# Optimization experiments

Hardware: AMD Instinct MI355X
Metric: run time of the kernel (lower is better)

Reference implementation:

```python
import jax, jax.numpy as jnp
import numpy as np

NV, NR = 30000, 1000
EVV, EVI, EIV = 400000, 120000, 120000
VD, RD, ED = 16, 8, 2
HID, OUT, H1 = 64, 64, 2


def _seg_softmax(logits, seg, n):
    # numerically stable segment softmax over destination nodes
    m = jax.ops.segment_max(logits, seg, num_segments=n)
    m = jnp.where(jnp.isfinite(m), m, 0.0)
    ex = jnp.exp(logits - m[seg])
    den = jax.ops.segment_sum(ex, seg, num_segments=n)
    return ex / (den[seg] + 1e-16)


def _gatv2(x_src, x_dst, src, dst, ea, Wl, Wr, We, att, b, heads, n_dst, concat):
    # PyG GATv2Conv: e = att . leaky_relu(Wl x_j + Wr x_i + We e_ij); out = sum_j softmax(e) * Wl x_j
    C = att.shape[-1]
    hl = (x_src @ Wl).reshape(-1, heads, C)
    hr = (x_dst @ Wr).reshape(-1, heads, C)
    he = (ea @ We).reshape(-1, heads, C)
    xj = hl[src]                                   # [E, H, C]
    g = jax.nn.leaky_relu(xj + hr[dst] + he, 0.2)
    logits = jnp.einsum('ehc,hc->eh', g, att)      # [E, H]
    alpha = _seg_softmax(logits, dst, n_dst)
    out = jax.ops.segment_sum(xj * alpha[..., None], dst, num_segments=n_dst)
    out = out.reshape(n_dst, heads * C) if concat else out.mean(axis=1)
    return out + b


def _self_loops(src, dst, ea, n):
    # PyG add_self_loops(fill_value='mean'): self-loop edge_attr = per-dst mean of incoming edge_attr
    deg = jax.ops.segment_sum(jnp.ones((ea.shape[0],), ea.dtype), dst, num_segments=n)
    mean = jax.ops.segment_sum(ea, dst, num_segments=n) / jnp.maximum(deg, 1.0)[:, None]
    ar = jnp.arange(n, dtype=src.dtype)
    return jnp.concatenate([src, ar]), jnp.concatenate([dst, ar]), jnp.concatenate([ea, mean], axis=0)


def _ln(x, g, b):
    m = x.mean(-1, keepdims=True)
    v = ((x - m) ** 2).mean(-1, keepdims=True)
    return (x - m) * jax.lax.rsqrt(v + 1e-5) * g + b


def setup_inputs() -> dict:
    key = jax.random.key(0)
    ks = iter(jax.random.split(key, 80))
    def rn(shape, s=1.0):
        return jax.random.normal(next(ks), shape, jnp.float32) * s
    def ri(n, hi):
        return jax.random.randint(next(ks), (n,), 0, hi, jnp.int32)
    d = {'x_veh': rn((NV, VD)), 'x_rsu': rn((NR, RD)),
         'ea_v2v': rn((EVV, ED)), 'ea_v2i': rn((EVI, ED)), 'ea_i2v': rn((EIV, ED)),
         'src_v2v': ri(EVV, NV), 'dst_v2v': ri(EVV, NV),
         'src_v2i': ri(EVI, NV), 'dst_v2i': ri(EVI, NR),
         'src_i2v': ri(EIV, NR), 'dst_i2v': ri(EIV, NV)}
    H1C = H1 * HID
    for rel, di_s, di_d in (('vv', VD, VD), ('vi', VD, RD), ('iv', RD, VD)):
        d['Wl_' + rel + '1'] = rn((di_s, H1C), 0.1)
        d['Wr_' + rel + '1'] = rn((di_d, H1C), 0.1)
        d['We_' + rel + '1'] = rn((ED, H1C), 0.1)
        d['att_' + rel + '1'] = rn((H1, HID), 0.1)
        d['b_' + rel + '1'] = jnp.zeros((H1C,), jnp.float32)
    for rel in ('vv', 'vi', 'iv'):
        d['Wl_' + rel + '2'] = rn((H1C, OUT), 0.1)
        d['Wr_' + rel + '2'] = rn((H1C, OUT), 0.1)
        d['We_' + rel + '2'] = rn((ED, OUT), 0.1)
        d['att_' + rel + '2'] = rn((1, OUT), 0.1)
        d['b_' + rel + '2'] = jnp.zeros((OUT,), jnp.float32)
    d['ln_vg'] = jnp.ones((OUT,), jnp.float32)
    d['ln_vb'] = jnp.zeros((OUT,), jnp.float32)
    d['ln_rg'] = jnp.ones((OUT,), jnp.float32)
    d['ln_rb'] = jnp.zeros((OUT,), jnp.float32)
    return d


def reference(x_veh, x_rsu, ea_v2v, ea_v2i, ea_i2v,
              src_v2v, dst_v2v, src_v2i, dst_v2i, src_i2v, dst_i2v,
              Wl_vv1, Wr_vv1, We_vv1, att_vv1, b_vv1,
              Wl_vi1, Wr_vi1, We_vi1, att_vi1, b_vi1,
              Wl_iv1, Wr_iv1, We_iv1, att_iv1, b_iv1,
              Wl_vv2, Wr_vv2, We_vv2, att_vv2, b_vv2,
              Wl_vi2, Wr_vi2, We_vi2, att_vi2, b_vi2,
              Wl_iv2, Wr_iv2, We_iv2, att_iv2, b_iv2,
              ln_vg, ln_vb, ln_rg, ln_rb):
    s_vv, d_vv, ea_vv = _self_loops(src_v2v, dst_v2v, ea_v2v, NV)
    # layer 1 (heads=2, concat=True), HeteroConv aggr='sum'
    v1 = (_gatv2(x_veh, x_veh, s_vv, d_vv, ea_vv, Wl_vv1, Wr_vv1, We_vv1, att_vv1, b_vv1, H1, NV, True)
          + _gatv2(x_rsu, x_veh, src_i2v, dst_i2v, ea_i2v, Wl_iv1, Wr_iv1, We_iv1, att_iv1, b_iv1, H1, NV, True))
    r1 = _gatv2(x_veh, x_rsu, src_v2i, dst_v2i, ea_v2i, Wl_vi1, Wr_vi1, We_vi1, att_vi1, b_vi1, H1, NR, True)
    v1 = jax.nn.elu(v1)
    r1 = jax.nn.elu(r1)
    # layer 2 (heads=1, concat=False -> mean over 1 head)
    v2 = (_gatv2(v1, v1, s_vv, d_vv, ea_vv, Wl_vv2, Wr_vv2, We_vv2, att_vv2, b_vv2, 1, NV, False)
          + _gatv2(r1, v1, src_i2v, dst_i2v, ea_i2v, Wl_iv2, Wr_iv2, We_iv2, att_iv2, b_iv2, 1, NV, False))
    r2 = _gatv2(v1, r1, src_v2i, dst_v2i, ea_v2i, Wl_vi2, Wr_vi2, We_vi2, att_vi2, b_vi2, 1, NR, False)
    return jnp.concatenate([_ln(v2, ln_vg, ln_vb), _ln(r2, ln_rg, ln_rb)], axis=0)
```

## Files before the change

kernel.cpp:

```cpp
#include <hip/hip_runtime.h>
#include <hip/hip_fp16.h>

constexpr int NV = 30000, NR = 1000;
constexpr int EVV = 400000, EVI = 120000, EIV = 120000;
constexpr int ETOT = EVV + EIV + EVI;
constexpr int VB = (NV + 3) / 4;

struct __align__(8) Edge { int s; __half2 ea; };
typedef __half2 h2;

__device__ __forceinline__ h2 h2shfl_xor(h2 v, int m) {
  int i = *(int*)&v;
  i = __shfl_xor(i, m);
  return *(h2*)&i;
}
__device__ __forceinline__ h2 h2max(h2 a, h2 b) {
  h2 r;
  asm("v_pk_max_f16 %0, %1, %2" : "=v"(r) : "v"(a), "v"(b));
  return r;
}

constexpr size_t OFF_CNT_VV = 0;
constexpr size_t OFF_CUR_VV = OFF_CNT_VV + NV;
constexpr size_t OFF_CNT_IV = OFF_CUR_VV + NV;
constexpr size_t OFF_CUR_IV = OFF_CNT_IV + NV;
constexpr size_t OFF_CNT_VI = OFF_CUR_IV + NV;
constexpr size_t OFF_CUR_VI = OFF_CNT_VI + NR;
constexpr size_t ZERO_END   = OFF_CUR_VI + NR;
constexpr size_t OFF_PTR_VV = ZERO_END;
constexpr size_t OFF_PTR_IV = OFF_PTR_VV + NV + 2;
constexpr size_t OFF_PTR_VI = OFF_PTR_IV + NV + 2;
constexpr size_t OFF_E_VV   = OFF_PTR_VI + NR + 2;
constexpr size_t OFF_E_IV   = OFF_E_VV + (size_t)EVV * 2;
constexpr size_t OFF_E_VI   = OFF_E_IV + (size_t)EIV * 2;
constexpr size_t OFF_H      = (OFF_E_VI + (size_t)EVI * 2 + 3) & ~(size_t)3;
constexpr size_t OFF_HL_VV1 = OFF_H;
constexpr size_t OFF_HR_VV1 = OFF_HL_VV1 + (size_t)NV * 64;
constexpr size_t OFF_HR_IV1 = OFF_HR_VV1 + (size_t)NV * 64;
constexpr size_t OFF_HL_VI1 = OFF_HR_IV1 + (size_t)NV * 64;
constexpr size_t OFF_HL_IV1 = OFF_HL_VI1 + (size_t)NV * 64;
constexpr size_t OFF_HR_VI1 = OFF_HL_IV1 + (size_t)NR * 64;
constexpr size_t L1_END     = OFF_HR_VI1 + (size_t)NR * 64;
constexpr size_t OFF_V1     = L1_END;
constexpr size_t OFF_R1     = OFF_V1 + (size_t)NV * 64;
constexpr size_t WS_END     = OFF_R1 + (size_t)NR * 64;
constexpr size_t OFF_HL_VV2 = OFF_H;
constexpr size_t OFF_HR_VV2 = OFF_HL_VV2 + (size_t)NV * 32;
constexpr size_t OFF_HR_IV2 = OFF_HR_VV2 + (size_t)NV * 32;
constexpr size_t OFF_HL_VI2 = OFF_HR_IV2 + (size_t)NV * 32;
constexpr size_t OFF_HL_IV2 = OFF_HL_VI2 + (size_t)NV * 32;
constexpr size_t OFF_HR_VI2 = OFF_HL_IV2 + (size_t)NR * 32;
constexpr size_t L2_END     = OFF_HR_VI2 + (size_t)NR * 32;
static_assert(L2_END <= OFF_V1, "layer-2 overlay must not clobber v1/r1");

__global__ __launch_bounds__(256) void k_count3(
    const int* __restrict__ dvv, const int* __restrict__ div_, const int* __restrict__ dvi,
    int* __restrict__ cvv, int* __restrict__ civ, int* __restrict__ cvi) {
  int t = blockIdx.x * blockDim.x + threadIdx.x;
  if (t < EVV) atomicAdd(&cvv[dvv[t]], 1);
  else if (t < EVV + EIV) atomicAdd(&civ[div_[t - EVV]], 1);
  else if (t < ETOT) atomicAdd(&cvi[dvi[t - EVV - EIV]], 1);
}

__global__ __launch_bounds__(1024) void k_scan3(
    const int* c0, int* p0, int n0,
    const int* c1, int* p1, int n1,
    const int* c2, int* p2, int n2) {
  const int* cnt = blockIdx.x == 0 ? c0 : blockIdx.x == 1 ? c1 : c2;
  int* ptr = blockIdx.x == 0 ? p0 : blockIdx.x == 1 ? p1 : p2;
  int n = blockIdx.x == 0 ? n0 : blockIdx.x == 1 ? n1 : n2;
  __shared__ int tsum[1024];
  int t = threadIdx.x;
  int per = (n + 1023) >> 10;
  int base = t * per;
  int s = 0;
  for (int i = 0; i < per; i++) { int idx = base + i; if (idx < n) s += cnt[idx]; }
  tsum[t] = s;
  for (int off = 1; off < 1024; off <<= 1) {
    __syncthreads();
    int v = (t >= off) ? tsum[t - off] : 0;
    __syncthreads();
    tsum[t] += v;
  }
  __syncthreads();
  int run = tsum[t] - s;
  for (int i = 0; i < per; i++) {
    int idx = base + i;
    if (idx < n) { ptr[idx] = run; run += cnt[idx]; }
  }
  if (t == 1023) ptr[n] = tsum[1023];
}

__global__ __launch_bounds__(256) void k_fill3(
    const int* __restrict__ svv, const int* __restrict__ dvv, const float* __restrict__ eavv,
    const int* __restrict__ siv, const int* __restrict__ div_, const float* __restrict__ eaiv,
    const int* __restrict__ svi, const int* __restrict__ dvi, const float* __restrict__ eavi,
    const int* __restrict__ pvv, int* __restrict__ uvv, Edge* __restrict__ evv,
    const int* __restrict__ piv, int* __restrict__ uiv, Edge* __restrict__ eiv,
    const int* __restrict__ pvi, int* __restrict__ uvi, Edge* __restrict__ evi) {
  int t = blockIdx.x * blockDim.x + threadIdx.x;
  if (t < EVV) {
    int e = t, d = dvv[e];
    int idx = pvv[d] + atomicAdd(&uvv[d], 1);
    Edge ed; ed.s = svv[e]; ed.ea = __floats2half2_rn(eavv[2 * e], eavv[2 * e + 1]);
    evv[idx] = ed;
  } else if (t < EVV + EIV) {
    int e = t - EVV, d = div_[e];
    int idx = piv[d] + atomicAdd(&uiv[d], 1);
    Edge ed; ed.s = siv[e]; ed.ea = __floats2half2_rn(eaiv[2 * e], eaiv[2 * e + 1]);
    eiv[idx] = ed;
  } else if (t < ETOT) {
    int e = t - EVV - EIV, d = dvi[e];
    int idx = pvi[d] + atomicAdd(&uvi[d], 1);
    Edge ed; ed.s = svi[e]; ed.ea = __floats2half2_rn(eavi[2 * e], eavi[2 * e + 1]);
    evi[idx] = ed;
  }
}

template<int K, int NW>
__global__ __launch_bounds__(256) void k_gemm1(const float* __restrict__ X,
    const float* __restrict__ W0, const float* __restrict__ W1,
    const float* __restrict__ W2, const float* __restrict__ W3,
    __half* __restrict__ Y0, __half* __restrict__ Y1,
    __half* __restrict__ Y2, __half* __restrict__ Y3, int n) {
  constexpr int ROWS = 8;
  __shared__ float xs[ROWS][K];
  int r0 = blockIdx.x * ROWS;
  int tid = threadIdx.x;
  int col = tid & 127, grp = tid >> 7;
  for (int i = tid; i < ROWS * K; i += 256) {
    int gi = r0 * K + i;
    ((float*)xs)[i] = (gi < n * K) ? X[gi] : 0.f;
  }
  __syncthreads();
  int oidx = ((col & 63) << 1) + (col >> 6);
#pragma unroll
  for (int rep = 0; rep < NW / 2; rep++) {
    int wi = grp + rep * 2;
    const float* __restrict__ W = wi == 0 ? W0 : wi == 1 ? W1 : wi == 2 ? W2 : W3;
    __half* __restrict__ Y = wi == 0 ? Y0 : wi == 1 ? Y1 : wi == 2 ? Y2 : Y3;
    float acc[ROWS];
#pragma unroll
    for (int r = 0; r < ROWS; r++) acc[r] = 0.f;
#pragma unroll
    for (int k4 = 0; k4 < K / 4; k4++) {
      float w0 = W[(4 * k4 + 0) * 128 + col];
      float w1 = W[(4 * k4 + 1) * 128 + col];
      float w2 = W[(4 * k4 + 2) * 128 + col];
      float w3 = W[(4 * k4 + 3) * 128 + col];
#pragma unroll
      for (int r = 0; r < ROWS; r++) {
        float4 x4 = *(const float4*)&xs[r][4 * k4];
        acc[r] = fmaf(x4.x, w0, acc[r]);
        acc[r] = fmaf(x4.y, w1, acc[r]);
        acc[r] = fmaf(x4.z, w2, acc[r]);
        acc[r] = fmaf(x4.w, w3, acc[r]);
      }
    }
#pragma unroll
    for (int r = 0; r < ROWS; r++)
      if (r0 + r < n) Y[(size_t)(r0 + r) * 128 + oidx] = __float2half(acc[r]);
  }
}

template<int NW>
__global__ __launch_bounds__(64 * NW) void k_gemm2(const __half* __restrict__ X,
    const float* __restrict__ W0, const float* __restrict__ W1,
    const float* __restrict__ W2, const float* __restrict__ W3,
    __half* __restrict__ Y0, __half* __restrict__ Y1,
    __half* __restrict__ Y2, __half* __restrict__ Y3, int n) {
  constexpr int ROWS = 16, K = 128;
  __shared__ float xs[ROWS][K];
  int r0 = blockIdx.x * ROWS;
  int tid = threadIdx.x;
  const __half2* X2 = (const __half2*)X;
  for (int i = tid; i < ROWS * K / 2; i += 64 * NW) {
    int gi = r0 * (K / 2) + i;
    float2 f = (gi < n * (K / 2)) ? __half22float2(X2[gi]) : make_float2(0.f, 0.f);
    ((float*)xs)[2 * i] = f.x;
    ((float*)xs)[2 * i + 1] = f.y;
  }
  __syncthreads();
  int lane = tid & 63, wv = tid >> 6;
  const float* __restrict__ W = wv == 0 ? W0 : wv == 1 ? W1 : wv == 2 ? W2 : W3;
  __half* __restrict__ Y = wv == 0 ? Y0 : wv == 1 ? Y1 : wv == 2 ? Y2 : Y3;
  float acc[ROWS];
#pragma unroll
  for (int r = 0; r < ROWS; r++) acc[r] = 0.f;
  for (int k4 = 0; k4 < K / 4; k4++) {
    float w0 = W[(4 * k4 + 0) * 64 + lane];
    float w1 = W[(4 * k4 + 1) * 64 + lane];
    float w2 = W[(4 * k4 + 2) * 64 + lane];
    float w3 = W[(4 * k4 + 3) * 64 + lane];
#pragma unroll
    for (int r = 0; r < ROWS; r++) {
      float4 x4 = *(const float4*)&xs[r][4 * k4];
      acc[r] = fmaf(x4.x, w0, acc[r]);
      acc[r] = fmaf(x4.y, w1, acc[r]);
      acc[r] = fmaf(x4.z, w2, acc[r]);
      acc[r] = fmaf(x4.w, w3, acc[r]);
    }
  }
#pragma unroll
  for (int r = 0; r < ROWS; r++)
    if (r0 + r < n) Y[(size_t)(r0 + r) * 64 + lane] = __float2half(acc[r]);
}


template<bool SELF>
__device__ __forceinline__ void gatW2(int d, int lane, int eg, int cg,
    int b, int cnt,
    const Edge* __restrict__ ed,
    const __half* __restrict__ hl, const __half* __restrict__ hr,
    const float* __restrict__ We, const float* __restrict__ att,
    float* acc, float& den0, float& den1) {
  h2 hrc2[4], av2[4], w02[4], w12[4];
  {
    float4 r = *(const float4*)&hr[(size_t)d * 128 + cg * 8];
    const h2* hp = (const h2*)&r;
#pragma unroll
    for (int j = 0; j < 4; j++) hrc2[j] = hp[j];
  }
#pragma unroll
  for (int j = 0; j < 4; j++) {
    int c = cg * 4 + j;
    av2[j] = __floats2half2_rn(att[c], att[64 + c]);
    w02[j] = __floats2half2_rn(We[c], We[64 + c]);
    w12[j] = __floats2half2_rn(We[128 + c], We[192 + c]);
  }
  const h2 c02 = __float2half2_rn(0.2f);
  float sum0 = 0.f, sum1 = 0.f;
  auto proc = [&](float4 r, int eab, bool v) {
    const h2* hp = (const h2*)&r;
    h2 eh = *(h2*)&eab;
    h2 ef0 = __low2half2(eh), ef1 = __high2half2(eh);
    h2 lacc = __float2half2_rn(0.f);
#pragma unroll
    for (int j = 0; j < 4; j++) {
      h2 g = __hfma2(ef0, w02[j], __hadd2(hp[j], hrc2[j]));
      g = __hfma2(ef1, w12[j], g);
      h2 lr = h2max(g, __hmul2(c02, g));
      lacc = __hfma2(lr, av2[j], lacc);
    }
#pragma unroll
    for (int o = 1; o <= 8; o <<= 1) lacc = __hadd2(lacc, h2shfl_xor(lacc, o));
    float2 lf = __half22float2(lacc);
    float ex0 = v ? __expf(lf.x) : 0.f;
    float ex1 = v ? __expf(lf.y) : 0.f;
#pragma unroll
    for (int j = 0; j < 4; j++) {
      float2 f = __half22float2(hp[j]);
      acc[2 * j]     = fmaf(ex0, f.x, acc[2 * j]);
      acc[2 * j + 1] = fmaf(ex1, f.y, acc[2 * j + 1]);
    }
    den0 += ex0; den1 += ex1;
  };
  for (int wf = 0; wf < cnt; wf += 64) {
    int idx = wf + lane;
    int es = 0, eab = 0;
    if (idx < cnt) { Edge e = ed[b + idx]; es = e.s; eab = *(const int*)&e.ea; }
    if (SELF) {
      float2 f = __half22float2(*(h2*)&eab);
      sum0 += f.x; sum1 += f.y;
    }
    int wlen = min(64, cnt - wf);
    for (int kk = 0; kk < wlen; kk += 16) {
      int k0 = kk + eg, k1 = kk + 4 + eg, k2 = kk + 8 + eg, k3 = kk + 12 + eg;
      int s0 = __shfl(es, k0), ea0 = __shfl(eab, k0);
      int s1 = __shfl(es, k1), ea1 = __shfl(eab, k1);
      int s2 = __shfl(es, k2), ea2 = __shfl(eab, k2);
      int s3 = __shfl(es, k3), ea3 = __shfl(eab, k3);
      float4 r0 = *(const float4*)&hl[(size_t)s0 * 128 + cg * 8];
      float4 r1 = *(const float4*)&hl[(size_t)s1 * 128 + cg * 8];
      float4 r2 = *(const float4*)&hl[(size_t)s2 * 128 + cg * 8];
      float4 r3 = *(const float4*)&hl[(size_t)s3 * 128 + cg * 8];
      proc(r0, ea0, k0 < wlen);
      proc(r1, ea1, k1 < wlen);
      proc(r2, ea2, k2 < wlen);
      proc(r3, ea3, k3 < wlen);
    }
  }
  if (SELF) {
#pragma unroll
    for (int o = 1; o <= 32; o <<= 1) { sum0 += __shfl_xor(sum0, o); sum1 += __shfl_xor(sum1, o); }
    float dg = fmaxf((float)cnt, 1.f);
    __half2 mh = __floats2half2_rn(sum0 / dg, sum1 / dg);
    int meab = *(const int*)&mh;
    float4 rS = *(const float4*)&hl[(size_t)d * 128 + cg * 8];
    proc(rS, meab, eg == 0);
  }
#pragma unroll
  for (int o = 16; o <= 32; o <<= 1) {
#pragma unroll
    for (int j = 0; j < 8; j++) acc[j] += __shfl_xor(acc[j], o);
    den0 += __shfl_xor(den0, o);
    den1 += __shfl_xor(den1, o);
  }
}

template<bool SELF>
__device__ __forceinline__ void gatW1(int d, int lane, int eg8, int cg8,
    int b, int cnt,
    const Edge* __restrict__ ed,
    const __half* __restrict__ hl, const __half* __restrict__ hr,
    const float* __restrict__ We, const float* __restrict__ att,
    float* acc, float& den) {
  h2 hrc2[4], av2[4], w02[4], w12[4];
  {
    float4 r = *(const float4*)&hr[(size_t)d * 64 + cg8 * 8];
    const h2* hp = (const h2*)&r;
#pragma unroll
    for (int j = 0; j < 4; j++) hrc2[j] = hp[j];
  }
#pragma unroll
  for (int j = 0; j < 4; j++) {
    int c = cg8 * 8 + 2 * j;
    av2[j] = __floats2half2_rn(att[c], att[c + 1]);
    w02[j] = __floats2half2_rn(We[c], We[c + 1]);
    w12[j] = __floats2half2_rn(We[64 + c], We[64 + c + 1]);
  }
  const h2 c02 = __float2half2_rn(0.2f);
  float sum0 = 0.f, sum1 = 0.f;
  auto proc = [&](float4 r, int eab, bool v) {
    const h2* hp = (const h2*)&r;
    h2 eh = *(h2*)&eab;
    h2 ef0 = __low2half2(eh), ef1 = __high2half2(eh);
    h2 lacc = __float2half2_rn(0.f);
#pragma unroll
    for (int j = 0; j < 4; j++) {
      h2 g = __hfma2(ef0, w02[j], __hadd2(hp[j], hrc2[j]));
      g = __hfma2(ef1, w12[j], g);
      h2 lr = h2max(g, __hmul2(c02, g));
      lacc = __hfma2(lr, av2[j], lacc);
    }
#pragma unroll
    for (int o = 1; o <= 4; o <<= 1) lacc = __hadd2(lacc, h2shfl_xor(lacc, o));
    float2 lf = __half22float2(lacc);
    float ex = v ? __expf(lf.x + lf.y) : 0.f;
#pragma unroll
    for (int j = 0; j < 4; j++) {
      float2 f = __half22float2(hp[j]);
      acc[2 * j]     = fmaf(ex, f.x, acc[2 * j]);
      acc[2 * j + 1] = fmaf(ex, f.y, acc[2 * j + 1]);
    }
    den += ex;
  };
  for (int wf = 0; wf < cnt; wf += 64) {
    int idx = wf + lane;
    int es = 0, eab = 0;
    if (idx < cnt) { Edge e = ed[b + idx]; es = e.s; eab = *(const int*)&e.ea; }
    if (SELF) {
      float2 f = __half22float2(*(h2*)&eab);
      sum0 += f.x; sum1 += f.y;
    }
    int wlen = min(64, cnt - wf);
    for (int kk = 0; kk < wlen; kk += 32) {
      int k0 = kk + eg8, k1 = kk + 8 + eg8, k2 = kk + 16 + eg8, k3 = kk + 24 + eg8;
      int s0 = __shfl(es, k0), ea0 = __shfl(eab, k0);
      int s1 = __shfl(es, k1), ea1 = __shfl(eab, k1);
      int s2 = __shfl(es, k2), ea2 = __shfl(eab, k2);
      int s3 = __shfl(es, k3), ea3 = __shfl(eab, k3);
      float4 r0 = *(const float4*)&hl[(size_t)s0 * 64 + cg8 * 8];
      float4 r1 = *(const float4*)&hl[(size_t)s1 * 64 + cg8 * 8];
      float4 r2 = *(const float4*)&hl[(size_t)s2 * 64 + cg8 * 8];
      float4 r3 = *(const float4*)&hl[(size_t)s3 * 64 + cg8 * 8];
      proc(r0, ea0, k0 < wlen);
      proc(r1, ea1, k1 < wlen);
      proc(r2, ea2, k2 < wlen);
      proc(r3, ea3, k3 < wlen);
    }
  }
  if (SELF) {
#pragma unroll
    for (int o = 1; o <= 32; o <<= 1) { sum0 += __shfl_xor(sum0, o); sum1 += __shfl_xor(sum1, o); }
    float dg = fmaxf((float)cnt, 1.f);
    __half2 mh = __floats2half2_rn(sum0 / dg, sum1 / dg);
    int meab = *(const int*)&mh;
    float4 rS = *(const float4*)&hl[(size_t)d * 64 + cg8 * 8];
    proc(rS, meab, eg8 == 0);
  }
#pragma unroll
  for (int o = 8; o <= 32; o <<= 1) {
#pragma unroll
    for (int j = 0; j < 8; j++) acc[j] += __shfl_xor(acc[j], o);
    den += __shfl_xor(den, o);
  }
}

__global__ __launch_bounds__(256) void k_gat_l1(
    const int* ptr_vv, const Edge* e_vv,
    const __half* hl_vv, const __half* hr_vv, const float* We_vv, const float* att_vv,
    const int* ptr_iv, const Edge* e_iv,
    const __half* hl_iv, const __half* hr_iv, const float* We_iv, const float* att_iv,
    const int* ptr_vi, const Edge* e_vi,
    const __half* hl_vi, const __half* hr_vi, const float* We_vi, const float* att_vi,
    const float* b_vv, const float* b_iv, const float* b_vi,
    __half* __restrict__ v1, __half* __restrict__ r1) {
  __shared__ float sm[4][16][10];
  int lane = threadIdx.x & 63, wv = threadIdx.x >> 6;
  int eg = lane >> 4, cg = lane & 15;
  if (blockIdx.x >= NR) {
    int w = (blockIdx.x - NR) * 4 + wv;
    if (w >= NV) return;
    float acc[8] = {0, 0, 0, 0, 0, 0, 0, 0};
    float d0 = 0.f, d1 = 0.f, oc[8];
    int b = ptr_vv[w], cnt = ptr_vv[w + 1] - b;
    gatW2<true>(w, lane, eg, cg, b, cnt, e_vv, hl_vv, hr_vv, We_vv, att_vv, acc, d0, d1);
#pragma unroll
    for (int j = 0; j < 8; j++) oc[j] = acc[j] / (((j & 1) ? d1 : d0) + 1e-16f);
#pragma unroll
    for (int j = 0; j < 8; j++) acc[j] = 0.f;
    d0 = d1 = 0.f;
    b = ptr_iv[w]; cnt = ptr_iv[w + 1] - b;
    gatW2<false>(w, lane, eg, cg, b, cnt, e_iv, hl_iv, hr_iv, We_iv, att_iv, acc, d0, d1);
#pragma unroll
    for (int j = 0; j < 8; j++) oc[j] += acc[j] / (((j & 1) ? d1 : d0) + 1e-16f);
    if (eg == 0) {
      float x[8];
#pragma unroll
      for (int j = 0; j < 8; j++) {
        int c = cg * 4 + (j >> 1);
        int idx = (j & 1) * 64 + c;
        float v = oc[j] + b_vv[idx] + b_iv[idx];
        x[j] = v > 0.f ? v : __expf(v) - 1.f;
      }
      __half2 h0a = __floats2half2_rn(x[0], x[2]), h0b = __floats2half2_rn(x[4], x[6]);
      __half2 h1a = __floats2half2_rn(x[1], x[3]), h1b = __floats2half2_rn(x[5], x[7]);
      float2 p0, p1;
      ((__half2*)&p0)[0] = h0a; ((__half2*)&p0)[1] = h0b;
      ((__half2*)&p1)[0] = h1a; ((__half2*)&p1)[1] = h1b;
      *(float2*)&v1[(size_t)w * 128 + cg * 4]      = p0;
      *(float2*)&v1[(size_t)w * 128 + 64 + cg * 4] = p1;
    }
  } else {
    int dd = blockIdx.x;
    int bfull = ptr_vi[dd], cntf = ptr_vi[dd + 1] - bfull;
    int q = (cntf + 3) >> 2;
    int off = min(wv * q, cntf);
    int cnt = min(q, cntf - off);
    float acc[8] = {0, 0, 0, 0, 0, 0, 0, 0};
    float d0 = 0.f, d1 = 0.f;
    gatW2<false>(dd, lane, eg, cg, bfull + off, cnt, e_vi, hl_vi, hr_vi, We_vi, att_vi, acc, d0, d1);
    if (eg == 0) {
#pragma unroll
      for (int j = 0; j < 8; j++) sm[wv][cg][j] = acc[j];
      sm[wv][cg][8] = d0; sm[wv][cg][9] = d1;
    }
    __syncthreads();
    if (wv == 0) {
#pragma unroll
      for (int j = 0; j < 8; j++)
        acc[j] = sm[0][cg][j] + sm[1][cg][j] + sm[2][cg][j] + sm[3][cg][j];
      d0 = sm[0][cg][8] + sm[1][cg][8] + sm[2][cg][8] + sm[3][cg][8];
      d1 = sm[0][cg][9] + sm[1][cg][9] + sm[2][cg][9] + sm[3][cg][9];
      if (eg == 0) {
        float x[8];
#pragma unroll
        for (int j = 0; j < 8; j++) {
          int c = cg * 4 + (j >> 1);
          int idx = (j & 1) * 64 + c;
          float v = acc[j] / (((j & 1) ? d1 : d0) + 1e-16f) + b_vi[idx];
          x[j] = v > 0.f ? v : __expf(v) - 1.f;
        }
        __half2 h0a = __floats2half2_rn(x[0], x[2]), h0b = __floats2half2_rn(x[4], x[6]);
        __half2 h1a = __floats2half2_rn(x[1], x[3]), h1b = __floats2half2_rn(x[5], x[7]);
        float2 p0, p1;
        ((__half2*)&p0)[0] = h0a; ((__half2*)&p0)[1] = h0b;
        ((__half2*)&p1)[0] = h1a; ((__half2*)&p1)[1] = h1b;
        *(float2*)&r1[(size_t)dd * 128 + cg * 4]      = p0;
        *(float2*)&r1[(size_t)dd * 128 + 64 + cg * 4] = p1;
      }
    }
  }
}

__global__ __launch_bounds__(256) void k_gat_l2(
    const int* ptr_vv, const Edge* e_vv,
    const __half* hl_vv, const __half* hr_vv, const float* We_vv, const float* att_vv,
    const int* ptr_iv, const Edge* e_iv,
    const __half* hl_iv, const __half* hr_iv, const float* We_iv, const float* att_iv,
    const int* ptr_vi, const Edge* e_vi,
    const __half* hl_vi, const __half* hr_vi, const float* We_vi, const float* att_vi,
    const float* b_vv, const float* b_iv, const float* b_vi,
    const float* ln_vg, const float* ln_vb, const float* ln_rg, const float* ln_rb,
    float* __restrict__ out) {
  __shared__ float sm[4][8][9];
  int lane = threadIdx.x & 63, wv = threadIdx.x >> 6;
  int eg8 = lane >> 3, cg8 = lane & 7;
  if (blockIdx.x >= NR) {
    int w = (blockIdx.x - NR) * 4 + wv;
    if (w >= NV) return;
    float acc[8] = {0, 0, 0, 0, 0, 0, 0, 0};
    float dn = 0.f, oc[8];
    int b = ptr_vv[w], cnt = ptr_vv[w + 1] - b;
    gatW1<true>(w, lane, eg8, cg8, b, cnt, e_vv, hl_vv, hr_vv, We_vv, att_vv, acc, dn);
#pragma unroll
    for (int j = 0; j < 8; j++) oc[j] = acc[j] / (dn + 1e-16f);
#pragma unroll
    for (int j = 0; j < 8; j++) acc[j] = 0.f;
    dn = 0.f;
    b = ptr_iv[w]; cnt = ptr_iv[w + 1] - b;
    gatW1<false>(w, lane, eg8, cg8, b, cnt, e_iv, hl_iv, hr_iv, We_iv, att_iv, acc, dn);
    float x[8], s = 0.f;
#pragma unroll
    for (int j = 0; j < 8; j++) {
      int c = cg8 * 8 + j;
      x[j] = oc[j] + acc[j] / (dn + 1e-16f) + b_vv[c] + b_iv[c];
      s += x[j];
    }
#pragma unroll
    for (int o = 1; o <= 4; o <<= 1) s += __shfl_xor(s, o);
    float mu = s * (1.f / 64.f);
    float v = 0.f;
#pragma unroll
    for (int j = 0; j < 8; j++) { float dx = x[j] - mu; v = fmaf(dx, dx, v); }
#pragma unroll
    for (int o = 1; o <= 4; o <<= 1) v += __shfl_xor(v, o);
    float rstd = rsqrtf(v * (1.f / 64.f) + 1e-5f);
    if (eg8 == 0) {
      float4 o0, o1;
      float* ov = (float*)&o0;
#pragma unroll
      for (int j = 0; j < 4; j++) {
        int c = cg8 * 8 + j;
        ov[j] = (x[j] - mu) * rstd * ln_vg[c] + ln_vb[c];
      }
      ov = (float*)&o1;
#pragma unroll
      for (int j = 0; j < 4; j++) {
        int c = cg8 * 8 + 4 + j;
        ov[j] = (x[4 + j] - mu) * rstd * ln_vg[c] + ln_vb[c];
      }
      *(float4*)&out[(size_t)w * 64 + cg8 * 8]     = o0;
      *(float4*)&out[(size_t)w * 64 + cg8 * 8 + 4] = o1;
    }
  } else {
    int dd = blockIdx.x;
    int bfull = ptr_vi[dd], cntf = ptr_vi[dd + 1] - bfull;
    int q = (cntf + 3) >> 2;
    int off = min(wv * q, cntf);
    int cnt = min(q, cntf - off);
    float acc[8] = {0, 0, 0, 0, 0, 0, 0, 0};
    float dn = 0.f;
    gatW1<false>(dd, lane, eg8, cg8, bfull + off, cnt, e_vi, hl_vi, hr_vi, We_vi, att_vi, acc, dn);
    if (eg8 == 0) {
#pragma unroll
      for (int j = 0; j < 8; j++) sm[wv][cg8][j] = acc[j];
      sm[wv][cg8][8] = dn;
    }
    __syncthreads();
    if (wv == 0) {
#pragma unroll
      for (int j = 0; j < 8; j++)
        acc[j] = sm[0][cg8][j] + sm[1][cg8][j] + sm[2][cg8][j] + sm[3][cg8][j];
      dn = sm[0][cg8][8] + sm[1][cg8][8] + sm[2][cg8][8] + sm[3][cg8][8];
      float x[8], s = 0.f;
#pragma unroll
      for (int j = 0; j < 8; j++) {
        int c = cg8 * 8 + j;
        x[j] = acc[j] / (dn + 1e-16f) + b_vi[c];
        s += x[j];
      }
#pragma unroll
      for (int o = 1; o <= 4; o <<= 1) s += __shfl_xor(s, o);
      float mu = s * (1.f / 64.f);
      float v = 0.f;
#pragma unroll
      for (int j = 0; j < 8; j++) { float dx = x[j] - mu; v = fmaf(dx, dx, v); }
#pragma unroll
      for (int o = 1; o <= 4; o <<= 1) v += __shfl_xor(v, o);
      float rstd = rsqrtf(v * (1.f / 64.f) + 1e-5f);
      if (eg8 == 0) {
#pragma unroll
        for (int j = 0; j < 8; j++) {
          int c = cg8 * 8 + j;
          out[(size_t)(NV + dd) * 64 + c] = (x[j] - mu) * rstd * ln_rg[c] + ln_rb[c];
        }
      }
    }
  }
}

extern "C" void kernel_launch(void* const* d_in, const int* in_sizes, int n_in,
                              void* d_out, int out_size, void* d_ws, size_t ws_size,
                              hipStream_t stream) {
  const float* x_veh  = (const float*)d_in[0];
  const float* x_rsu  = (const float*)d_in[1];
  const float* ea_vv  = (const float*)d_in[2];
  const float* ea_vi  = (const float*)d_in[3];
  const float* ea_iv  = (const float*)d_in[4];
  const int*   src_vv = (const int*)d_in[5];
  const int*   dst_vv = (const int*)d_in[6];
  const int*   src_vi = (const int*)d_in[7];
  const int*   dst_vi = (const int*)d_in[8];
  const int*   src_iv = (const int*)d_in[9];
  const int*   dst_iv = (const int*)d_in[10];
  const float* Wl_vv1 = (const float*)d_in[11];
  const float* Wr_vv1 = (const float*)d_in[12];
  const float* We_vv1 = (const float*)d_in[13];
  const float* att_vv1= (const float*)d_in[14];
  const float* b_vv1  = (const float*)d_in[15];
  const float* Wl_vi1 = (const float*)d_in[16];
  const float* Wr_vi1 = (const float*)d_in[17];
  const float* We_vi1 = (const float*)d_in[18];
  const float* att_vi1= (const float*)d_in[19];
  const float* b_vi1  = (const float*)d_in[20];
  const float* Wl_iv1 = (const float*)d_in[21];
  const float* Wr_iv1 = (const float*)d_in[22];
  const float* We_iv1 = (const float*)d_in[23];
  const float* att_iv1= (const float*)d_in[24];
  const float* b_iv1  = (const float*)d_in[25];
  const float* Wl_vv2 = (const float*)d_in[26];
  const float* Wr_vv2 = (const float*)d_in[27];
  const float* We_vv2 = (const float*)d_in[28];
  const float* att_vv2= (const float*)d_in[29];
  const float* b_vv2  = (const float*)d_in[30];
  const float* Wl_vi2 = (const float*)d_in[31];
  const float* Wr_vi2 = (const float*)d_in[32];
  const float* We_vi2 = (const float*)d_in[33];
  const float* att_vi2= (const float*)d_in[34];
  const float* b_vi2  = (const float*)d_in[35];
  const float* Wl_iv2 = (const float*)d_in[36];
  const float* Wr_iv2 = (const float*)d_in[37];
  const float* We_iv2 = (const float*)d_in[38];
  const float* att_iv2= (const float*)d_in[39];
  const float* b_iv2  = (const float*)d_in[40];
  const float* ln_vg  = (const float*)d_in[41];
  const float* ln_vb  = (const float*)d_in[42];
  const float* ln_rg  = (const float*)d_in[43];
  const float* ln_rb  = (const float*)d_in[44];

  float* ws  = (float*)d_ws;
  float* out = (float*)d_out;

  int* cnt_vv = (int*)(ws + OFF_CNT_VV); int* cur_vv = (int*)(ws + OFF_CUR_VV);
  int* cnt_iv = (int*)(ws + OFF_CNT_IV); int* cur_iv = (int*)(ws + OFF_CUR_IV);
  int* cnt_vi = (int*)(ws + OFF_CNT_VI); int* cur_vi = (int*)(ws + OFF_CUR_VI);
  int* ptr_vv = (int*)(ws + OFF_PTR_VV);
  int* ptr_iv = (int*)(ws + OFF_PTR_IV);
  int* ptr_vi = (int*)(ws + OFF_PTR_VI);
  Edge* e_vv = (Edge*)(ws + OFF_E_VV);
  Edge* e_iv = (Edge*)(ws + OFF_E_IV);
  Edge* e_vi = (Edge*)(ws + OFF_E_VI);

  __half* hl_vv1 = (__half*)(ws + OFF_HL_VV1);
  __half* hr_vv1 = (__half*)(ws + OFF_HR_VV1);
  __half* hr_iv1 = (__half*)(ws + OFF_HR_IV1);
  __half* hl_vi1 = (__half*)(ws + OFF_HL_VI1);
  __half* hl_iv1 = (__half*)(ws + OFF_HL_IV1);
  __half* hr_vi1 = (__half*)(ws + OFF_HR_VI1);
  __half* v1 = (__half*)(ws + OFF_V1);
  __half* r1 = (__half*)(ws + OFF_R1);
  __half* hl_vv2 = (__half*)(ws + OFF_HL_VV2);
  __half* hr_vv2 = (__half*)(ws + OFF_HR_VV2);
  __half* hr_iv2 = (__half*)(ws + OFF_HR_IV2);
  __half* hl_vi2 = (__half*)(ws + OFF_HL_VI2);
  __half* hl_iv2 = (__half*)(ws + OFF_HL_IV2);
  __half* hr_vi2 = (__half*)(ws + OFF_HR_VI2);

  (void)hipMemsetAsync(ws, 0, ZERO_END * sizeof(float), stream);

  k_count3<<<(ETOT + 255) / 256, 256, 0, stream>>>(dst_vv, dst_iv, dst_vi,
      cnt_vv, cnt_iv, cnt_vi);
  k_scan3<<<3, 1024, 0, stream>>>(cnt_vv, ptr_vv, NV, cnt_iv, ptr_iv, NV, cnt_vi, ptr_vi, NR);
  k_fill3<<<(ETOT + 255) / 256, 256, 0, stream>>>(
      src_vv, dst_vv, ea_vv, src_iv, dst_iv, ea_iv, src_vi, dst_vi, ea_vi,
      ptr_vv, cur_vv, e_vv, ptr_iv, cur_iv, e_iv, ptr_vi, cur_vi, e_vi);

  k_gemm1<16, 4><<<(NV + 7) / 8, 256, 0, stream>>>(x_veh,
      Wl_vv1, Wr_vv1, Wr_iv1, Wl_vi1, hl_vv1, hr_vv1, hr_iv1, hl_vi1, NV);
  k_gemm1<8, 2><<<(NR + 7) / 8, 256, 0, stream>>>(x_rsu,
      Wl_iv1, Wr_vi1, nullptr, nullptr, hl_iv1, hr_vi1, nullptr, nullptr, NR);

  k_gat_l1<<<NR + VB, 256, 0, stream>>>(
      ptr_vv, e_vv, hl_vv1, hr_vv1, We_vv1, att_vv1,
      ptr_iv, e_iv, hl_iv1, hr_iv1, We_iv1, att_iv1,
      ptr_vi, e_vi, hl_vi1, hr_vi1, We_vi1, att_vi1,
      b_vv1, b_iv1, b_vi1, v1, r1);

  k_gemm2<4><<<(NV + 15) / 16, 256, 0, stream>>>(v1,
      Wl_vv2, Wr_vv2, Wr_iv2, Wl_vi2, hl_vv2, hr_vv2, hr_iv2, hl_vi2, NV);
  k_gemm2<2><<<(NR + 15) / 16, 128, 0, stream>>>(r1,
      Wl_iv2, Wr_vi2, nullptr, nullptr, hl_iv2, hr_vi2, nullptr, nullptr, NR);

  k_gat_l2<<<NR + VB, 256, 0, stream>>>(
      ptr_vv, e_vv, hl_vv2, hr_vv2, We_vv2, att_vv2,
      ptr_iv, e_iv, hl_iv2, hr_iv2, We_iv2, att_iv2,
      ptr_vi, e_vi, hl_vi2, hr_vi2, We_vi2, att_vi2,
      b_vv2, b_iv2, b_vi2, ln_vg, ln_vb, ln_rg, ln_rb, out);
  (void)in_sizes; (void)n_in; (void)out_size; (void)ws_size;
}
```

Measured before the change: 365.0 us.

## Accumulate weighted messages in packed fp16 and split edge loop into full and tail

The per-edge weighted accumulation of source features moves from eight fp32 FMAs to four packed fp16 FMAs. The exponent is shifted by a constant offset so the fp16 accumulators stay in range, and the cross-lane reduction now shuffles half2 values. The edge loop is split into an unpredicated main body that handles four edges per group and a one-edge tail, which cuts the validity checks. This lowers ALU and register cost in the aggregation, but fp16 accumulation can lose precision or overflow on high-degree nodes or large logits.

```diff
diff --git a/kernel.cpp b/kernel.cpp
--- a/kernel.cpp
+++ b/kernel.cpp
@@ -5,6 +5,7 @@
 constexpr int EVV = 400000, EVI = 120000, EIV = 120000;
 constexpr int ETOT = EVV + EIV + EVI;
 constexpr int VB = (NV + 3) / 4;
+constexpr float LOFF = 4.0f;
 
 struct __align__(8) Edge { int s; __half2 ea; };
 typedef __half2 h2;
@@ -229,6 +230,9 @@
     w12[j] = __floats2half2_rn(We[128 + c], We[192 + c]);
   }
   const h2 c02 = __float2half2_rn(0.2f);
+  h2 acc2[4];
+#pragma unroll
+  for (int j = 0; j < 4; j++) acc2[j] = __float2half2_rn(0.f);
   float sum0 = 0.f, sum1 = 0.f;
   auto proc = [&](float4 r, int eab, bool v) {
     const h2* hp = (const h2*)&r;
@@ -245,14 +249,11 @@
 #pragma unroll
     for (int o = 1; o <= 8; o <<= 1) lacc = __hadd2(lacc, h2shfl_xor(lacc, o));
     float2 lf = __half22float2(lacc);
-    float ex0 = v ? __expf(lf.x) : 0.f;
-    float ex1 = v ? __expf(lf.y) : 0.f;
-#pragma unroll
-    for (int j = 0; j < 4; j++) {
-      float2 f = __half22float2(hp[j]);
-      acc[2 * j]     = fmaf(ex0, f.x, acc[2 * j]);
-      acc[2 * j + 1] = fmaf(ex1, f.y, acc[2 * j + 1]);
-    }
+    float ex0 = v ? __expf(lf.x - LOFF) : 0.f;
+    float ex1 = v ? __expf(lf.y - LOFF) : 0.f;
+    h2 exh = __floats2half2_rn(ex0, ex1);
+#pragma unroll
+    for (int j = 0; j < 4; j++) acc2[j] = __hfma2(exh, hp[j], acc2[j]);
     den0 += ex0; den1 += ex1;
   };
   for (int wf = 0; wf < cnt; wf += 64) {
@@ -264,7 +265,8 @@
       sum0 += f.x; sum1 += f.y;
     }
     int wlen = min(64, cnt - wf);
-    for (int kk = 0; kk < wlen; kk += 16) {
+    int kk = 0;
+    for (; kk + 16 <= wlen; kk += 16) {
       int k0 = kk + eg, k1 = kk + 4 + eg, k2 = kk + 8 + eg, k3 = kk + 12 + eg;
       int s0 = __shfl(es, k0), ea0 = __shfl(eab, k0);
       int s1 = __shfl(es, k1), ea1 = __shfl(eab, k1);
@@ -274,10 +276,16 @@
       float4 r1 = *(const float4*)&hl[(size_t)s1 * 128 + cg * 8];
       float4 r2 = *(const float4*)&hl[(size_t)s2 * 128 + cg * 8];
       float4 r3 = *(const float4*)&hl[(size_t)s3 * 128 + cg * 8];
+      proc(r0, ea0, true);
+      proc(r1, ea1, true);
+      proc(r2, ea2, true);
+      proc(r3, ea3, true);
+    }
+    for (; kk < wlen; kk += 4) {
+      int k0 = kk + eg;
+      int s0 = __shfl(es, k0), ea0 = __shfl(eab, k0);
+      float4 r0 = *(const float4*)&hl[(size_t)s0 * 128 + cg * 8];
       proc(r0, ea0, k0 < wlen);
-      proc(r1, ea1, k1 < wlen);
-      proc(r2, ea2, k2 < wlen);
-      proc(r3, ea3, k3 < wlen);
     }
   }
   if (SELF) {
@@ -292,9 +300,14 @@
 #pragma unroll
   for (int o = 16; o <= 32; o <<= 1) {
 #pragma unroll
-    for (int j = 0; j < 8; j++) acc[j] += __shfl_xor(acc[j], o);
+    for (int j = 0; j < 4; j++) acc2[j] = __hadd2(acc2[j], h2shfl_xor(acc2[j], o));
     den0 += __shfl_xor(den0, o);
     den1 += __shfl_xor(den1, o);
+  }
+#pragma unroll
+  for (int j = 0; j < 4; j++) {
+    float2 f = __half22float2(acc2[j]);
+    acc[2 * j] = f.x; acc[2 * j + 1] = f.y;
   }
 }
 
@@ -320,6 +333,9 @@
     w12[j] = __floats2half2_rn(We[64 + c], We[64 + c + 1]);
   }
   const h2 c02 = __float2half2_rn(0.2f);
+  h2 acc2[4];
+#pragma unroll
+  for (int j = 0; j < 4; j++) acc2[j] = __float2half2_rn(0.f);
   float sum0 = 0.f, sum1 = 0.f;
   auto proc = [&](float4 r, int eab, bool v) {
     const h2* hp = (const h2*)&r;
@@ -336,13 +352,10 @@
 #pragma unroll
     for (int o = 1; o <= 4; o <<= 1) lacc = __hadd2(lacc, h2shfl_xor(lacc, o));
     float2 lf = __half22float2(lacc);
-    float ex = v ? __expf(lf.x + lf.y) : 0.f;
-#pragma unroll
-    for (int j = 0; j < 4; j++) {
-      float2 f = __half22float2(hp[j]);
-      acc[2 * j]     = fmaf(ex, f.x, acc[2 * j]);
-      acc[2 * j + 1] = fmaf(ex, f.y, acc[2 * j + 1]);
-    }
+    float ex = v ? __expf(lf.x + lf.y - LOFF) : 0.f;
+    h2 exh = __float2half2_rn(ex);
+#pragma unroll
+    for (int j = 0; j < 4; j++) acc2[j] = __hfma2(exh, hp[j], acc2[j]);
     den += ex;
   };
   for (int wf = 0; wf < cnt; wf += 64) {
@@ -354,7 +367,8 @@
       sum0 += f.x; sum1 += f.y;
     }
     int wlen = min(64, cnt - wf);
-    for (int kk = 0; kk < wlen; kk += 32) {
+    int kk = 0;
+    for (; kk + 32 <= wlen; kk += 32) {
       int k0 = kk + eg8, k1 = kk + 8 + eg8, k2 = kk + 16 + eg8, k3 = kk + 24 + eg8;
       int s0 = __shfl(es, k0), ea0 = __shfl(eab, k0);
       int s1 = __shfl(es, k1), ea1 = __shfl(eab, k1);
@@ -364,10 +378,16 @@
       float4 r1 = *(const float4*)&hl[(size_t)s1 * 64 + cg8 * 8];
       float4 r2 = *(const float4*)&hl[(size_t)s2 * 64 + cg8 * 8];
       float4 r3 = *(const float4*)&hl[(size_t)s3 * 64 + cg8 * 8];
+      proc(r0, ea0, true);
+      proc(r1, ea1, true);
+      proc(r2, ea2, true);
+      proc(r3, ea3, true);
+    }
+    for (; kk < wlen; kk += 8) {
+      int k0 = kk + eg8;
+      int s0 = __shfl(es, k0), ea0 = __shfl(eab, k0);
+      float4 r0 = *(const float4*)&hl[(size_t)s0 * 64 + cg8 * 8];
       proc(r0, ea0, k0 < wlen);
-      proc(r1, ea1, k1 < wlen);
-      proc(r2, ea2, k2 < wlen);
-      proc(r3, ea3, k3 < wlen);
     }
   }
   if (SELF) {
@@ -382,8 +402,13 @@
 #pragma unroll
   for (int o = 8; o <= 32; o <<= 1) {
 #pragma unroll
-    for (int j = 0; j < 8; j++) acc[j] += __shfl_xor(acc[j], o);
+    for (int j = 0; j < 4; j++) acc2[j] = __hadd2(acc2[j], h2shfl_xor(acc2[j], o));
     den += __shfl_xor(den, o);
+  }
+#pragma unroll
+  for (int j = 0; j < 4; j++) {
+    float2 f = __half22float2(acc2[j]);
+    acc[2 * j] = f.x; acc[2 * j + 1] = f.y;
   }
 }
 
@@ -402,14 +427,12 @@
   if (blockIdx.x >= NR) {
     int w = (blockIdx.x - NR) * 4 + wv;
     if (w >= NV) return;
-    float acc[8] = {0, 0, 0, 0, 0, 0, 0, 0};
+    float acc[8];
     float d0 = 0.f, d1 = 0.f, oc[8];
     int b = ptr_vv[w], cnt = ptr_vv[w + 1] - b;
     gatW2<true>(w, lane, eg, cg, b, cnt, e_vv, hl_vv, hr_vv, We_vv, att_vv, acc, d0, d1);
 #pragma unroll
     for (int j = 0; j < 8; j++) oc[j] = acc[j] / (((j & 1) ? d1 : d0) + 1e-16f);
-#pragma unroll
-    for (int j = 0; j < 8; j++) acc[j] = 0.f;
     d0 = d1 = 0.f;
     b = ptr_iv[w]; cnt = ptr_iv[w + 1] - b;
     gatW2<false>(w, lane, eg, cg, b, cnt, e_iv, hl_iv, hr_iv, We_iv, att_iv, acc, d0, d1);
@@ -438,7 +461,7 @@
     int q = (cntf + 3) >> 2;
     int off = min(wv * q, cntf);
     int cnt = min(q, cntf - off);
-    float acc[8] = {0, 0, 0, 0, 0, 0, 0, 0};
+    float acc[8];
     float d0 = 0.f, d1 = 0.f;
     gatW2<false>(dd, lane, eg, cg, bfull + off, cnt, e_vi, hl_vi, hr_vi, We_vi, att_vi, acc, d0, d1);
     if (eg == 0) {
@@ -490,14 +513,12 @@
   if (blockIdx.x >= NR) {
     int w = (blockIdx.x - NR) * 4 + wv;
     if (w >= NV) return;
-    float acc[8] = {0, 0, 0, 0, 0, 0, 0, 0};
+    float acc[8];
     float dn = 0.f, oc[8];
     int b = ptr_vv[w], cnt = ptr_vv[w + 1] - b;
     gatW1<true>(w, lane, eg8, cg8, b, cnt, e_vv, hl_vv, hr_vv, We_vv, att_vv, acc, dn);
 #pragma unroll
     for (int j = 0; j < 8; j++) oc[j] = acc[j] / (dn + 1e-16f);
-#pragma unroll
-    for (int j = 0; j < 8; j++) acc[j] = 0.f;
     dn = 0.f;
     b = ptr_iv[w]; cnt = ptr_iv[w + 1] - b;
     gatW1<false>(w, lane, eg8, cg8, b, cnt, e_iv, hl_iv, hr_iv, We_iv, att_iv, acc, dn);
@@ -540,7 +561,7 @@
     int q = (cntf + 3) >> 2;
     int off = min(wv * q, cntf);
     int cnt = min(q, cntf - off);
-    float acc[8] = {0, 0, 0, 0, 0, 0, 0, 0};
+    float acc[8];
     float dn = 0.f;
     gatW1<false>(dd, lane, eg8, cg8, bfull + off, cnt, e_vi, hl_vi, hr_vi, We_vi, att_vi, acc, dn);
     if (eg8 == 0) {
```

New measurement: 360.2 us. Within noise of the previous version (-1.3%).
